# Kernel optimization log

Hardware: AMD Instinct MI355X
Metric: run time of the kernel (lower is better)

## Reference

```python
import jax, jax.numpy as jnp
import numpy as np

TOPK = 2  # top_k from __init__


def setup_inputs() -> dict:
    key = jax.random.key(0)
    k0, k1, k2, k3 = jax.random.split(key, 4)
    B, D, DFF, E = 8192, 1024, 1024, 32
    scale = 0.02
    return {
        "moe_inp": jax.random.normal(k0, (B, D), jnp.float32),
        "wg": jax.random.normal(k1, (D, E), jnp.float32) * scale,
        "bg": jnp.zeros((E,), jnp.float32),
        "w1": jax.random.normal(k2, (E, D, DFF), jnp.float32) * scale,
        "b1": jnp.zeros((E, DFF), jnp.float32),
        "w2": jax.random.normal(k3, (E, DFF, D), jnp.float32) * scale,
        "b2": jnp.zeros((E, D), jnp.float32),
    }


def reference(moe_inp, wg, bg, w1, b1, w2, b2):
    E = wg.shape[1]
    B = moe_inp.shape[0]
    # --- NaiveGate: linear -> top_k -> softmax over selected logits ---
    logits = moe_inp @ wg + bg                      # [B, E]
    top_val, gate_top_k_idx = jax.lax.top_k(logits, TOPK)  # [B, TOPK]
    gate_score = jax.nn.softmax(top_val, axis=-1)   # computed by gate; NOT applied
    # to expert outputs in pMoE's forward (combine is a plain sum), kept faithful.
    del gate_score
    # --- prepare_balance_forward: stable counting sort of token->expert slots ---
    gate_flat = gate_top_k_idx.reshape(-1)          # [B*TOPK] expert id per slot
    pos = jnp.argsort(gate_flat, stable=True)       # expert-sorted slot order
    fwd_expert_count = jnp.bincount(gate_flat, length=E).astype(jnp.int32)  # [E]
    # --- MoEReshape dispatch: gather token features into expert-contiguous rows ---
    x_disp = moe_inp[pos // TOPK]                   # [B*TOPK, D]
    eid = gate_flat[pos]                            # expert id per dispatched row
    # --- fused expert FFN: grouped GEMM per expert (variable-size batches) ---
    h = jax.lax.ragged_dot(x_disp, w1, fwd_expert_count) + b1[eid]  # [B*TOPK, DFF]
    h = jax.nn.gelu(h, approximate=False)
    y = jax.lax.ragged_dot(h, w2, fwd_expert_count) + b2[eid]       # [B*TOPK, D]
    # --- combine: view as [*, TOPK, D], sum topk dim, truncate to batch ---
    reduced = y.reshape(-1, TOPK, y.shape[-1]).sum(axis=1)          # [B, D]
    moe_outp = reduced[:B]
    return moe_outp, gate_top_k_idx
```

## Files before the change

### kernel.cpp

```cpp
#include <hip/hip_runtime.h>
#include <hip/hip_bf16.h>
#include <math.h>

#define NTOK 8192
#define DMODEL 1024
#define NEXP 32

typedef __attribute__((ext_vector_type(8))) short bf16x8;
typedef __attribute__((ext_vector_type(4))) float f32x4;

__device__ __forceinline__ unsigned int pk_bf16(float a, float b) {
  __hip_bfloat162 h = __float22bfloat162_rn(make_float2(a, b));
  union { __hip_bfloat162 h2; unsigned int u; } cv;
  cv.h2 = h;
  return cv.u;
}

__device__ __forceinline__ void gl_lds16(const unsigned short* g, unsigned short* l) {
  __builtin_amdgcn_global_load_lds(
      (const __attribute__((address_space(1))) unsigned int*)g,
      (__attribute__((address_space(3))) unsigned int*)l, 16, 0, 0);
}

__global__ __launch_bounds__(256) void convert_x(const float* __restrict__ x,
                                                 unsigned short* __restrict__ xb) {
  size_t i = (size_t)(blockIdx.x * 256 + threadIdx.x) * 8;
  float4 f0 = *reinterpret_cast<const float4*>(x + i);
  float4 f1 = *reinterpret_cast<const float4*>(x + i + 4);
  uint4 d;
  d.x = pk_bf16(f0.x, f0.y);
  d.y = pk_bf16(f0.z, f0.w);
  d.z = pk_bf16(f1.x, f1.y);
  d.w = pk_bf16(f1.z, f1.w);
  *reinterpret_cast<uint4*>(xb + i) = d;
}

__global__ __launch_bounds__(256) void transpose_cvt2(const float* __restrict__ w,
                                                      unsigned short* __restrict__ wt) {
  int bid = blockIdx.x;
  int e = bid >> 8;
  int tk = (bid >> 4) & 15;
  int tn = bid & 15;
  const float* src = w + ((size_t)e << 20) + ((size_t)(tk * 64) << 10) + tn * 64;
  unsigned short* dst = wt + ((size_t)e << 20) + ((size_t)(tn * 64) << 10) + tk * 64;
  __shared__ unsigned int Ts[64 * 32];
  int t = threadIdx.x;
  {
    int kp = t >> 3;
    int c8 = t & 7;
    const float* s0 = src + (size_t)(2 * kp) * 1024 + c8 * 8;
    float4 a0 = *reinterpret_cast<const float4*>(s0);
    float4 a1 = *reinterpret_cast<const float4*>(s0 + 4);
    float4 b0 = *reinterpret_cast<const float4*>(s0 + 1024);
    float4 b1 = *reinterpret_cast<const float4*>(s0 + 1028);
    float av[8] = {a0.x, a0.y, a0.z, a0.w, a1.x, a1.y, a1.z, a1.w};
    float bv[8] = {b0.x, b0.y, b0.z, b0.w, b1.x, b1.y, b1.z, b1.w};
#pragma unroll
    for (int i = 0; i < 8; i++) {
      int n = c8 * 8 + i;
      Ts[n * 32 + (kp ^ (n & 28))] = pk_bf16(av[i], bv[i]);
    }
  }
  __syncthreads();
  {
    int n = t >> 2;
    int kq = t & 3;
#pragma unroll
    for (int h = 0; h < 2; h++) {
      int k4 = kq + h * 4;
      int phys4 = (4 * k4) ^ (n & 28);
      uint4 d = *reinterpret_cast<const uint4*>(&Ts[n * 32 + phys4]);
      *reinterpret_cast<uint4*>(dst + (size_t)n * 1024 + k4 * 8) = d;
    }
  }
}

__global__ __launch_bounds__(256) void gate_partial(
    const float* __restrict__ x, const float* __restrict__ wg,
    float* __restrict__ partial) {
  __shared__ float Xs[256 * 20];
  int tid = threadIdx.x;
  int part = blockIdx.x >> 5;
  int tb = blockIdx.x & 31;
  int d0 = part * 128;
  float acc[32];
#pragma unroll
  for (int e = 0; e < 32; e++) acc[e] = 0.f;
  for (int ck = 0; ck < 8; ck++) {
    __syncthreads();
#pragma unroll
    for (int q = 0; q < 4; q++) {
      int li = q * 256 + tid;
      int row = li >> 2, j = li & 3;
      float4 v = *reinterpret_cast<const float4*>(
          x + (size_t)(tb * 256 + row) * DMODEL + d0 + ck * 16 + j * 4);
      *reinterpret_cast<float4*>(&Xs[row * 20 + j * 4]) = v;
    }
    __syncthreads();
#pragma unroll
    for (int d4 = 0; d4 < 4; d4++) {
      float4 xv = *reinterpret_cast<const float4*>(&Xs[tid * 20 + d4 * 4]);
      float xs[4] = {xv.x, xv.y, xv.z, xv.w};
#pragma unroll
      for (int dd = 0; dd < 4; dd++) {
        int d = d0 + ck * 16 + d4 * 4 + dd;
#pragma unroll
        for (int e = 0; e < 32; e++) acc[e] += xs[dd] * wg[d * 32 + e];
      }
    }
  }
  float* dst = partial + ((size_t)part * NTOK + tb * 256 + tid) * 32;
#pragma unroll
  for (int e = 0; e < 32; e += 4)
    *reinterpret_cast<float4*>(dst + e) =
        make_float4(acc[e], acc[e + 1], acc[e + 2], acc[e + 3]);
}

__global__ __launch_bounds__(256) void gate_top2(
    const float* __restrict__ partial, const float* __restrict__ bg,
    float* __restrict__ idx_out, int* __restrict__ eid,
    int* __restrict__ counts) {
  int t = blockIdx.x * 256 + threadIdx.x;
  float l[32];
#pragma unroll
  for (int e = 0; e < 32; e++) l[e] = bg[e];
  for (int p = 0; p < 8; p++) {
    const float* src = partial + ((size_t)p * NTOK + t) * 32;
#pragma unroll
    for (int e = 0; e < 32; e += 4) {
      float4 v = *reinterpret_cast<const float4*>(src + e);
      l[e] += v.x; l[e + 1] += v.y; l[e + 2] += v.z; l[e + 3] += v.w;
    }
  }
  int i0 = 0; float v0 = l[0];
#pragma unroll
  for (int e = 1; e < 32; e++)
    if (l[e] > v0) { v0 = l[e]; i0 = e; }
  int i1 = -1; float v1 = -3.0e38f;
#pragma unroll
  for (int e = 0; e < 32; e++)
    if (e != i0 && l[e] > v1) { v1 = l[e]; i1 = e; }
  *reinterpret_cast<float2*>(idx_out + t * 2) = make_float2((float)i0, (float)i1);
  eid[t * 2] = i0;
  eid[t * 2 + 1] = i1;
  atomicAdd(&counts[i0], 1);
  atomicAdd(&counts[i1], 1);
}

__global__ void scan_k(const int* __restrict__ counts, int* __restrict__ offsets) {
  if (threadIdx.x == 0) {
    int s = 0;
    for (int e = 0; e < 32; e++) { offsets[e] = s; s += counts[e]; }
    offsets[32] = s;
  }
}

__global__ __launch_bounds__(256) void build_stable(
    const int* __restrict__ eid, const int* __restrict__ offsets,
    int* __restrict__ tok_list) {
  int e = blockIdx.x;
  int tid = threadIdx.x;
  int lane = tid & 63, wv = tid >> 6;
  __shared__ int wcnt[4];
  int base = offsets[e];
  for (int c = 0; c < 64; c++) {
    int s = c * 256 + tid;
    bool f = (eid[s] == e);
    unsigned long long m = __ballot(f);
    if (lane == 0) wcnt[wv] = __popcll(m);
    __syncthreads();
    int woff = 0;
#pragma unroll
    for (int i = 0; i < 4; i++) woff += (i < wv) ? wcnt[i] : 0;
    int tot = wcnt[0] + wcnt[1] + wcnt[2] + wcnt[3];
    if (f) {
      int rank = woff + __popcll(m & ((1ull << lane) - 1ull));
      tok_list[base + rank] = s >> 1;
    }
    base += tot;
    __syncthreads();
  }
}

template <int PHASE>
__global__ __launch_bounds__(512, 4) void moe_gemm3(
    const unsigned short* __restrict__ Wt, const float* __restrict__ bias,
    const unsigned short* __restrict__ Ain, unsigned short* __restrict__ Hout,
    float* __restrict__ out, const int* __restrict__ tok_list,
    const int* __restrict__ offsets, const int* __restrict__ counts) {
  int bx = blockIdx.x;
  int e = bx & 31;
  int mt = (bx >> 5) & 7;
  int nt = bx >> 8;
  int n_e = counts[e];
  int m0 = mt * 128;
  if (m0 >= n_e) return;
  int n0 = nt * 256;
  int seg = offsets[e];

  __shared__ __align__(16) unsigned short As[2][128 * 32];
  __shared__ __align__(16) unsigned short Bs[2][256 * 32];

  int tid = threadIdx.x, lane = tid & 63, wid = tid >> 6;
  int wm = (wid >> 2) * 64, wn = (wid & 3) * 64;
  int ml = lane & 15, q = lane >> 4;

  int arow = wid * 16 + (lane >> 2);
  int agr = m0 + arow;
  int acr = (agr < n_e) ? agr : (n_e - 1);
  int atok = (PHASE == 0) ? tok_list[seg + acr] : (seg + acr);
  size_t a_off = (size_t)atok * DMODEL + (((lane & 3) ^ (arow & 3)) * 8);
  size_t b_off[2];
#pragma unroll
  for (int p = 0; p < 2; p++) {
    int brow = wid * 32 + p * 16 + (lane >> 2);
    b_off[p] = ((size_t)e * DMODEL + n0 + brow) * DMODEL +
               (((lane & 3) ^ (brow & 3)) * 8);
  }

  f32x4 acc[4][4];
#pragma unroll
  for (int im = 0; im < 4; im++)
#pragma unroll
    for (int in = 0; in < 4; in++) acc[im][in] = (f32x4){0.f, 0.f, 0.f, 0.f};

#define STAGE(BUF, K0)                                                \
  {                                                                   \
    gl_lds16(Ain + a_off + (K0), &As[BUF][wid * 512]);                \
    gl_lds16(Wt + b_off[0] + (K0), &Bs[BUF][(wid * 2) * 512]);        \
    gl_lds16(Wt + b_off[1] + (K0), &Bs[BUF][(wid * 2 + 1) * 512]);    \
  }

  STAGE(0, 0)
  STAGE(1, 32)

  for (int kt = 0; kt < 32; kt++) {
    int buf = kt & 1;
    if (kt < 31)
      asm volatile("s_waitcnt vmcnt(3)" ::: "memory");
    else
      asm volatile("s_waitcnt vmcnt(0)" ::: "memory");
    __builtin_amdgcn_s_barrier();

    bf16x8 af[4], bfr[4];
#pragma unroll
    for (int im = 0; im < 4; im++) {
      int r = wm + im * 16 + ml;
      af[im] = *reinterpret_cast<const bf16x8*>(
          &As[buf][r * 32 + ((q ^ (r & 3)) * 8)]);
    }
#pragma unroll
    for (int in = 0; in < 4; in++) {
      int r = wn + in * 16 + ml;
      bfr[in] = *reinterpret_cast<const bf16x8*>(
          &Bs[buf][r * 32 + ((q ^ (r & 3)) * 8)]);
    }
#pragma unroll
    for (int im = 0; im < 4; im++)
#pragma unroll
      for (int in = 0; in < 4; in++)
        acc[im][in] = __builtin_amdgcn_mfma_f32_16x16x32_bf16(
            af[im], bfr[in], acc[im][in], 0, 0, 0);

    asm volatile("s_waitcnt lgkmcnt(0)" ::: "memory");
    __builtin_amdgcn_s_barrier();
    if (kt < 30) {
      int k0 = (kt + 2) * 32;
      STAGE(buf, k0)
    }
  }
#undef STAGE

#pragma unroll
  for (int in = 0; in < 4; in++) {
    int n = n0 + wn + in * 16 + ml;
    float bv = bias[e * DMODEL + n];
#pragma unroll
    for (int im = 0; im < 4; im++) {
      int mb = m0 + wm + im * 16 + q * 4;
      if (PHASE == 0) {
#pragma unroll
        for (int r = 0; r < 4; r++) {
          int gr = mb + r;
          if (gr < n_e) {
            float v = acc[im][in][r] + bv;
            float g = 0.5f * v * (1.f + erff(v * 0.70710678118654752f));
            Hout[(size_t)(seg + gr) * DMODEL + n] =
                (unsigned short)(__hip_bfloat16_raw(__float2bfloat16(g)).x);
          }
        }
      } else {
        float v[4];
        bool ok[4];
#pragma unroll
        for (int r = 0; r < 4; r++) {
          ok[r] = (mb + r) < n_e;
          v[r] = acc[im][in][r] + bv;
        }
        int dp0 = seg + mb;
        if ((seg & 1) == 0) {
#pragma unroll
          for (int r = 0; r < 4; r += 2) {
            if (ok[r] && ok[r + 1])
              atomicAdd(out + (size_t)((dp0 + r) >> 1) * DMODEL + n,
                        v[r] + v[r + 1]);
            else {
              if (ok[r]) atomicAdd(out + (size_t)((dp0 + r) >> 1) * DMODEL + n, v[r]);
              if (ok[r + 1])
                atomicAdd(out + (size_t)((dp0 + r + 1) >> 1) * DMODEL + n, v[r + 1]);
            }
          }
        } else {
          if (ok[0]) atomicAdd(out + (size_t)(dp0 >> 1) * DMODEL + n, v[0]);
          if (ok[1] && ok[2])
            atomicAdd(out + (size_t)((dp0 + 1) >> 1) * DMODEL + n, v[1] + v[2]);
          else {
            if (ok[1]) atomicAdd(out + (size_t)((dp0 + 1) >> 1) * DMODEL + n, v[1]);
            if (ok[2]) atomicAdd(out + (size_t)((dp0 + 2) >> 1) * DMODEL + n, v[2]);
          }
          if (ok[3]) atomicAdd(out + (size_t)((dp0 + 3) >> 1) * DMODEL + n, v[3]);
        }
      }
    }
  }
}

extern "C" void kernel_launch(void* const* d_in, const int* in_sizes, int n_in,
                              void* d_out, int out_size, void* d_ws,
                              size_t ws_size, hipStream_t stream) {
  const float* x  = (const float*)d_in[0];
  const float* wg = (const float*)d_in[1];
  const float* bg = (const float*)d_in[2];
  const float* w1 = (const float*)d_in[3];
  const float* b1 = (const float*)d_in[4];
  const float* w2 = (const float*)d_in[5];
  const float* b2 = (const float*)d_in[6];
  float* out = (float*)d_out;

  char* w = (char*)d_ws;
  int* counts   = (int*)(w);
  int* offsets  = (int*)(w + 256);
  int* eid      = (int*)(w + 512);
  int* tok_list = (int*)(w + 512 + 65536);
  float* partial = (float*)(w + 131584);
  unsigned short* Hbuf = (unsigned short*)(w + 131584 + 8388608);
  unsigned short* Xb   = (unsigned short*)(w + 131584 + 8388608 + 33554432);
  unsigned short* w1t  = (unsigned short*)(w + 131584 + 8388608 + 33554432 + 16777216);
  unsigned short* w2t  = (unsigned short*)(w + 131584 + 8388608 + 33554432 + 16777216 + 67108864);

  hipMemsetAsync(d_ws, 0, 512, stream);
  hipMemsetAsync(d_out, 0, (size_t)NTOK * DMODEL * sizeof(float), stream);

  convert_x<<<dim3(4096), 256, 0, stream>>>(x, Xb);
  transpose_cvt2<<<dim3(8192), 256, 0, stream>>>(w1, w1t);
  transpose_cvt2<<<dim3(8192), 256, 0, stream>>>(w2, w2t);

  gate_partial<<<dim3(256), 256, 0, stream>>>(x, wg, partial);
  gate_top2<<<dim3(32), 256, 0, stream>>>(partial, bg, out + (size_t)NTOK * DMODEL,
                                          eid, counts);
  scan_k<<<1, 64, 0, stream>>>(counts, offsets);
  build_stable<<<dim3(32), 256, 0, stream>>>(eid, offsets, tok_list);

  moe_gemm3<0><<<dim3(1024), 512, 0, stream>>>(w1t, b1, Xb, Hbuf, nullptr,
                                               tok_list, offsets, counts);
  moe_gemm3<1><<<dim3(1024), 512, 0, stream>>>(w2t, b2, Hbuf, nullptr, out,
                                               tok_list, offsets, counts);
}
```

Baseline: 633.5 us.

## Enlarge grouped-GEMM M tile to 256 rows with split MFMA phases and setprio

Doubles the per-block M tile in both expert GEMMs from 128 to 256 rows. Each wave now holds an 8x4 accumulator grid, and the grid shrinks to 512 blocks. Each B (weight) tile loaded into LDS is therefore reused across twice as many token rows, cutting weight traffic. The MFMA loop is split into two halves with explicit lgkmcnt waits, sched_barrier and s_setprio to overlap LDS reads with matrix ops, and the LDS swizzle pattern is changed. In exchange it doubles accumulator registers and A-tile LDS per block under unchanged launch bounds, which risks spills or lower occupancy and worse tail utilisation for small experts.

```diff
diff --git a/kernel.cpp b/kernel.cpp
--- a/kernel.cpp
+++ b/kernel.cpp
@@ -190,45 +190,45 @@
     const int* __restrict__ offsets, const int* __restrict__ counts) {
   int bx = blockIdx.x;
   int e = bx & 31;
-  int mt = (bx >> 5) & 7;
-  int nt = bx >> 8;
+  int mt = (bx >> 5) & 3;
+  int nt = (bx >> 7) & 3;
   int n_e = counts[e];
-  int m0 = mt * 128;
+  int m0 = mt * 256;
   if (m0 >= n_e) return;
   int n0 = nt * 256;
   int seg = offsets[e];
 
-  __shared__ __align__(16) unsigned short As[2][128 * 32];
+  __shared__ __align__(16) unsigned short As[2][256 * 32];
   __shared__ __align__(16) unsigned short Bs[2][256 * 32];
 
   int tid = threadIdx.x, lane = tid & 63, wid = tid >> 6;
-  int wm = (wid >> 2) * 64, wn = (wid & 3) * 64;
+  int wm = (wid >> 2) * 128, wn = (wid & 3) * 64;
   int ml = lane & 15, q = lane >> 4;
 
-  int arow = wid * 16 + (lane >> 2);
-  int agr = m0 + arow;
-  int acr = (agr < n_e) ? agr : (n_e - 1);
-  int atok = (PHASE == 0) ? tok_list[seg + acr] : (seg + acr);
-  size_t a_off = (size_t)atok * DMODEL + (((lane & 3) ^ (arow & 3)) * 8);
-  size_t b_off[2];
-#pragma unroll
-  for (int p = 0; p < 2; p++) {
-    int brow = wid * 32 + p * 16 + (lane >> 2);
-    b_off[p] = ((size_t)e * DMODEL + n0 + brow) * DMODEL +
-               (((lane & 3) ^ (brow & 3)) * 8);
-  }
-
-  f32x4 acc[4][4];
-#pragma unroll
-  for (int im = 0; im < 4; im++)
+  size_t a_off[2], b_off[2];
+#pragma unroll
+  for (int j = 0; j < 2; j++) {
+    int arow = wid * 32 + j * 16 + (lane >> 2);
+    int agr = m0 + arow;
+    int acr = (agr < n_e) ? agr : (n_e - 1);
+    int atok = (PHASE == 0) ? tok_list[seg + acr] : (seg + acr);
+    int chunk = (lane & 3) ^ ((arow >> 1) & 3);
+    a_off[j] = (size_t)atok * DMODEL + chunk * 8;
+    b_off[j] = ((size_t)e * DMODEL + n0 + arow) * DMODEL + chunk * 8;
+  }
+
+  f32x4 acc[8][4];
+#pragma unroll
+  for (int im = 0; im < 8; im++)
 #pragma unroll
     for (int in = 0; in < 4; in++) acc[im][in] = (f32x4){0.f, 0.f, 0.f, 0.f};
 
-#define STAGE(BUF, K0)                                                \
-  {                                                                   \
-    gl_lds16(Ain + a_off + (K0), &As[BUF][wid * 512]);                \
-    gl_lds16(Wt + b_off[0] + (K0), &Bs[BUF][(wid * 2) * 512]);        \
-    gl_lds16(Wt + b_off[1] + (K0), &Bs[BUF][(wid * 2 + 1) * 512]);    \
+#define STAGE(BUF, K0)                                                  \
+  {                                                                     \
+    gl_lds16(Ain + a_off[0] + (K0), &As[BUF][(wid * 32) * 32]);         \
+    gl_lds16(Ain + a_off[1] + (K0), &As[BUF][(wid * 32 + 16) * 32]);    \
+    gl_lds16(Wt + b_off[0] + (K0), &Bs[BUF][(wid * 32) * 32]);          \
+    gl_lds16(Wt + b_off[1] + (K0), &Bs[BUF][(wid * 32 + 16) * 32]);     \
   }
 
   STAGE(0, 0)
@@ -237,32 +237,53 @@
   for (int kt = 0; kt < 32; kt++) {
     int buf = kt & 1;
     if (kt < 31)
-      asm volatile("s_waitcnt vmcnt(3)" ::: "memory");
+      asm volatile("s_waitcnt vmcnt(4)" ::: "memory");
     else
       asm volatile("s_waitcnt vmcnt(0)" ::: "memory");
     __builtin_amdgcn_s_barrier();
 
-    bf16x8 af[4], bfr[4];
+    bf16x8 bfr[4], af[4];
+#pragma unroll
+    for (int in = 0; in < 4; in++) {
+      int r = wn + in * 16 + ml;
+      bfr[in] = *reinterpret_cast<const bf16x8*>(
+          &Bs[buf][r * 32 + ((q ^ ((r >> 1) & 3)) * 8)]);
+    }
 #pragma unroll
     for (int im = 0; im < 4; im++) {
       int r = wm + im * 16 + ml;
       af[im] = *reinterpret_cast<const bf16x8*>(
-          &As[buf][r * 32 + ((q ^ (r & 3)) * 8)]);
-    }
-#pragma unroll
-    for (int in = 0; in < 4; in++) {
-      int r = wn + in * 16 + ml;
-      bfr[in] = *reinterpret_cast<const bf16x8*>(
-          &Bs[buf][r * 32 + ((q ^ (r & 3)) * 8)]);
-    }
+          &As[buf][r * 32 + ((q ^ ((r >> 1) & 3)) * 8)]);
+    }
+    asm volatile("s_waitcnt lgkmcnt(0)" ::: "memory");
+    __builtin_amdgcn_sched_barrier(0);
+    __builtin_amdgcn_s_setprio(1);
 #pragma unroll
     for (int im = 0; im < 4; im++)
 #pragma unroll
       for (int in = 0; in < 4; in++)
         acc[im][in] = __builtin_amdgcn_mfma_f32_16x16x32_bf16(
             af[im], bfr[in], acc[im][in], 0, 0, 0);
-
+    __builtin_amdgcn_s_setprio(0);
+
+    bf16x8 ag[4];
+#pragma unroll
+    for (int im = 0; im < 4; im++) {
+      int r = wm + 64 + im * 16 + ml;
+      ag[im] = *reinterpret_cast<const bf16x8*>(
+          &As[buf][r * 32 + ((q ^ ((r >> 1) & 3)) * 8)]);
+    }
     asm volatile("s_waitcnt lgkmcnt(0)" ::: "memory");
+    __builtin_amdgcn_sched_barrier(0);
+    __builtin_amdgcn_s_setprio(1);
+#pragma unroll
+    for (int im = 0; im < 4; im++)
+#pragma unroll
+      for (int in = 0; in < 4; in++)
+        acc[im + 4][in] = __builtin_amdgcn_mfma_f32_16x16x32_bf16(
+            ag[im], bfr[in], acc[im + 4][in], 0, 0, 0);
+    __builtin_amdgcn_s_setprio(0);
+
     __builtin_amdgcn_s_barrier();
     if (kt < 30) {
       int k0 = (kt + 2) * 32;
@@ -276,7 +297,7 @@
     int n = n0 + wn + in * 16 + ml;
     float bv = bias[e * DMODEL + n];
 #pragma unroll
-    for (int im = 0; im < 4; im++) {
+    for (int im = 0; im < 8; im++) {
       int mb = m0 + wm + im * 16 + q * 4;
       if (PHASE == 0) {
 #pragma unroll
@@ -361,8 +382,8 @@
   scan_k<<<1, 64, 0, stream>>>(counts, offsets);
   build_stable<<<dim3(32), 256, 0, stream>>>(eid, offsets, tok_list);
 
-  moe_gemm3<0><<<dim3(1024), 512, 0, stream>>>(w1t, b1, Xb, Hbuf, nullptr,
-                                               tok_list, offsets, counts);
-  moe_gemm3<1><<<dim3(1024), 512, 0, stream>>>(w2t, b2, Hbuf, nullptr, out,
-                                               tok_list, offsets, counts);
-}
+  moe_gemm3<0><<<dim3(512), 512, 0, stream>>>(w1t, b1, Xb, Hbuf, nullptr,
+                                              tok_list, offsets, counts);
+  moe_gemm3<1><<<dim3(512), 512, 0, stream>>>(w2t, b2, Hbuf, nullptr, out,
+                                              tok_list, offsets, counts);
+}
```

New measurement: 1.299 ms. +105.1%, slower.

## Fuse x bf16 conversion into gate kernel, widen build_stable, change LDS swizzle

Applied to the files above, without the earlier changes.

Removes the separate convert_x launch: gate_partial now writes the bf16 copy of x while it stages x tiles, which saves one full read of the fp32 input. build_stable runs 512 threads per block and 32 iterations instead of 256 threads and 64 iterations, which shortens its serial loop. The LDS XOR swizzle in the grouped GEMM now keys on (row>>1)&3 instead of row&3, to lower bank conflicts on the fragment reads. The extra 8-byte stores from gate_partial may coalesce poorly and slow that kernel down.

```diff
diff --git a/kernel.cpp b/kernel.cpp
--- a/kernel.cpp
+++ b/kernel.cpp
@@ -20,19 +20,6 @@
   __builtin_amdgcn_global_load_lds(
       (const __attribute__((address_space(1))) unsigned int*)g,
       (__attribute__((address_space(3))) unsigned int*)l, 16, 0, 0);
-}
-
-__global__ __launch_bounds__(256) void convert_x(const float* __restrict__ x,
-                                                 unsigned short* __restrict__ xb) {
-  size_t i = (size_t)(blockIdx.x * 256 + threadIdx.x) * 8;
-  float4 f0 = *reinterpret_cast<const float4*>(x + i);
-  float4 f1 = *reinterpret_cast<const float4*>(x + i + 4);
-  uint4 d;
-  d.x = pk_bf16(f0.x, f0.y);
-  d.y = pk_bf16(f0.z, f0.w);
-  d.z = pk_bf16(f1.x, f1.y);
-  d.w = pk_bf16(f1.z, f1.w);
-  *reinterpret_cast<uint4*>(xb + i) = d;
 }
 
 __global__ __launch_bounds__(256) void transpose_cvt2(const float* __restrict__ w,
@@ -77,7 +64,7 @@
 
 __global__ __launch_bounds__(256) void gate_partial(
     const float* __restrict__ x, const float* __restrict__ wg,
-    float* __restrict__ partial) {
+    float* __restrict__ partial, unsigned short* __restrict__ xb) {
   __shared__ float Xs[256 * 20];
   int tid = threadIdx.x;
   int part = blockIdx.x >> 5;
@@ -92,9 +79,12 @@
     for (int q = 0; q < 4; q++) {
       int li = q * 256 + tid;
       int row = li >> 2, j = li & 3;
+      int col = d0 + ck * 16 + j * 4;
       float4 v = *reinterpret_cast<const float4*>(
-          x + (size_t)(tb * 256 + row) * DMODEL + d0 + ck * 16 + j * 4);
+          x + (size_t)(tb * 256 + row) * DMODEL + col);
       *reinterpret_cast<float4*>(&Xs[row * 20 + j * 4]) = v;
+      uint2 d2 = make_uint2(pk_bf16(v.x, v.y), pk_bf16(v.z, v.w));
+      *reinterpret_cast<uint2*>(xb + (size_t)(tb * 256 + row) * DMODEL + col) = d2;
     }
     __syncthreads();
 #pragma unroll
@@ -155,24 +145,26 @@
   }
 }
 
-__global__ __launch_bounds__(256) void build_stable(
+__global__ __launch_bounds__(512) void build_stable(
     const int* __restrict__ eid, const int* __restrict__ offsets,
     int* __restrict__ tok_list) {
   int e = blockIdx.x;
   int tid = threadIdx.x;
   int lane = tid & 63, wv = tid >> 6;
-  __shared__ int wcnt[4];
+  __shared__ int wcnt[8];
   int base = offsets[e];
-  for (int c = 0; c < 64; c++) {
-    int s = c * 256 + tid;
+  for (int c = 0; c < 32; c++) {
+    int s = c * 512 + tid;
     bool f = (eid[s] == e);
     unsigned long long m = __ballot(f);
     if (lane == 0) wcnt[wv] = __popcll(m);
     __syncthreads();
     int woff = 0;
 #pragma unroll
-    for (int i = 0; i < 4; i++) woff += (i < wv) ? wcnt[i] : 0;
-    int tot = wcnt[0] + wcnt[1] + wcnt[2] + wcnt[3];
+    for (int i = 0; i < 8; i++) woff += (i < wv) ? wcnt[i] : 0;
+    int tot = 0;
+#pragma unroll
+    for (int i = 0; i < 8; i++) tot += wcnt[i];
     if (f) {
       int rank = woff + __popcll(m & ((1ull << lane) - 1ull));
       tok_list[base + rank] = s >> 1;
@@ -209,13 +201,13 @@
   int agr = m0 + arow;
   int acr = (agr < n_e) ? agr : (n_e - 1);
   int atok = (PHASE == 0) ? tok_list[seg + acr] : (seg + acr);
-  size_t a_off = (size_t)atok * DMODEL + (((lane & 3) ^ (arow & 3)) * 8);
+  size_t a_off = (size_t)atok * DMODEL + (((lane & 3) ^ ((arow >> 1) & 3)) * 8);
   size_t b_off[2];
 #pragma unroll
   for (int p = 0; p < 2; p++) {
     int brow = wid * 32 + p * 16 + (lane >> 2);
     b_off[p] = ((size_t)e * DMODEL + n0 + brow) * DMODEL +
-               (((lane & 3) ^ (brow & 3)) * 8);
+               (((lane & 3) ^ ((brow >> 1) & 3)) * 8);
   }
 
   f32x4 acc[4][4];
@@ -247,13 +239,13 @@
     for (int im = 0; im < 4; im++) {
       int r = wm + im * 16 + ml;
       af[im] = *reinterpret_cast<const bf16x8*>(
-          &As[buf][r * 32 + ((q ^ (r & 3)) * 8)]);
+          &As[buf][r * 32 + ((q ^ ((r >> 1) & 3)) * 8)]);
     }
 #pragma unroll
     for (int in = 0; in < 4; in++) {
       int r = wn + in * 16 + ml;
       bfr[in] = *reinterpret_cast<const bf16x8*>(
-          &Bs[buf][r * 32 + ((q ^ (r & 3)) * 8)]);
+          &Bs[buf][r * 32 + ((q ^ ((r >> 1) & 3)) * 8)]);
     }
 #pragma unroll
     for (int im = 0; im < 4; im++)
@@ -351,15 +343,14 @@
   hipMemsetAsync(d_ws, 0, 512, stream);
   hipMemsetAsync(d_out, 0, (size_t)NTOK * DMODEL * sizeof(float), stream);
 
-  convert_x<<<dim3(4096), 256, 0, stream>>>(x, Xb);
   transpose_cvt2<<<dim3(8192), 256, 0, stream>>>(w1, w1t);
   transpose_cvt2<<<dim3(8192), 256, 0, stream>>>(w2, w2t);
 
-  gate_partial<<<dim3(256), 256, 0, stream>>>(x, wg, partial);
+  gate_partial<<<dim3(256), 256, 0, stream>>>(x, wg, partial, Xb);
   gate_top2<<<dim3(32), 256, 0, stream>>>(partial, bg, out + (size_t)NTOK * DMODEL,
                                           eid, counts);
   scan_k<<<1, 64, 0, stream>>>(counts, offsets);
-  build_stable<<<dim3(32), 256, 0, stream>>>(eid, offsets, tok_list);
+  build_stable<<<dim3(32), 512, 0, stream>>>(eid, offsets, tok_list);
 
   moe_gemm3<0><<<dim3(1024), 512, 0, stream>>>(w1t, b1, Xb, Hbuf, nullptr,
                                                tok_list, offsets, counts);
```

After: 609.6 us. -3.8%, faster.
